# Optimization experiments

Measured on AMD Instinct MI355X. Metric: run time of the kernel, lower is better.

The kernel has to match this reference:

```python
import jax, jax.numpy as jnp
import numpy as np

B, CQ, CR, HID, H, W = 8, 1024, 512, 256, 48, 48


def setup_inputs() -> dict:
    key = jax.random.key(0)
    ks = jax.random.split(key, 6)
    return {
        "query_features": jax.random.normal(ks[0], (B, CQ, H, W), dtype=jnp.float32),
        "reference_features": jax.random.normal(ks[1], (B, CR, H, W), dtype=jnp.float32),
        "Wq": jax.random.normal(ks[2], (HID, CQ), dtype=jnp.float32) * (1.0 / np.sqrt(CQ)),
        "bq": jax.random.normal(ks[3], (HID,), dtype=jnp.float32) * 0.01,
        "Wk": jax.random.normal(ks[4], (HID, CR), dtype=jnp.float32) * (1.0 / np.sqrt(CR)),
        "bk": jax.random.normal(ks[5], (HID,), dtype=jnp.float32) * 0.01,
    }


def reference(query_features, reference_features, Wq, bq, Wk, bk):
    b, _, h1, w1 = query_features.shape
    h2, w2 = reference_features.shape[-2:]
    # 1x1 convs == per-pixel linear projections
    Q = jnp.einsum("oc,bchw->bohw", Wq, query_features) + bq[None, :, None, None]
    K = jnp.einsum("oc,bchw->bohw", Wk, reference_features) + bk[None, :, None, None]
    # V: [b, c_ref, h2*w2]
    V = reference_features.reshape(b, reference_features.shape[1], h2 * w2)
    # attention logits: [b, h1, w1, h2*w2]
    attn = jnp.einsum("bcij,bckl->bijkl", Q, K).reshape(b, h1, w1, h2 * w2)
    attn = jax.nn.softmax(attn, axis=3)
    # weighted sum of V: [b, c_ref, h1, w1]
    attended = jnp.einsum("bijp,bcp->bcij", attn, V)
    return attended
```

## Files before the change

kernel.cpp:

```cpp
#include <hip/hip_runtime.h>

#define BB   8
#define PP   2304
#define CQD  1024
#define CRD  512
#define HIDD 256
#define GB   4
#define NKB  36
#define LOG2E 1.4426950408889634f

typedef float f32x4 __attribute__((ext_vector_type(4)));
typedef __bf16 bf16x8 __attribute__((ext_vector_type(8)));
typedef unsigned short u16x8 __attribute__((ext_vector_type(8)));
typedef unsigned short u16x4 __attribute__((ext_vector_type(4)));
typedef unsigned int u32x4 __attribute__((ext_vector_type(4)));
typedef unsigned short ushort_t;

__device__ __forceinline__ unsigned short f2bf(float f) {
  unsigned int u = __float_as_uint(f);
  u += 0x7fffu + ((u >> 16) & 1u);
  return (unsigned short)(u >> 16);
}
__device__ __forceinline__ float bf2f(unsigned short h) {
  return __uint_as_float(((unsigned int)h) << 16);
}
__device__ __forceinline__ bf16x8 load_bf8(const ushort_t* p) {
  return *(const bf16x8*)p;
}
__device__ __forceinline__ void async16(const void* g, void* l) {
  __builtin_amdgcn_global_load_lds(
      (const __attribute__((address_space(1))) unsigned int*)g,
      (__attribute__((address_space(3))) unsigned int*)l, 16, 0, 0);
}

#define MFMA16(a, b, c) __builtin_amdgcn_mfma_f32_16x16x32_bf16((a), (b), (c), 0, 0, 0)

__global__ __launch_bounds__(256) void wcast_kernel(
    const float* __restrict__ W, ushort_t* __restrict__ Wh,
    ushort_t* __restrict__ Wl) {
  const size_t i = ((size_t)blockIdx.x * 256 + threadIdx.x) * 8;
  float4 a = *(const float4*)(W + i);
  float4 b2 = *(const float4*)(W + i + 4);
  float av[8] = {a.x, a.y, a.z, a.w, b2.x, b2.y, b2.z, b2.w};
  u16x8 h, l;
#pragma unroll
  for (int j = 0; j < 8; ++j) {
    unsigned short hh = f2bf(av[j]);
    h[j] = hh;
    l[j] = f2bf(av[j] - bf2f(hh));
  }
  *(u16x8*)(Wh + i) = h;
  *(u16x8*)(Wl + i) = l;
}

template <int C>
__global__ __launch_bounds__(256) void tcast_kernel(
    const float* __restrict__ X, ushort_t* __restrict__ Th,
    ushort_t* __restrict__ Tl) {
  const int b = blockIdx.z;
  const int p0 = blockIdx.x * 64;
  const int c0 = blockIdx.y * 64;
  const int tid = threadIdx.x;

  __shared__ unsigned int HL[64][66];

  {
    const int cr = tid >> 2;
    const int ch = tid & 3;
    const float* src = X + ((size_t)b * C + c0 + cr) * PP + p0 + ch * 16;
#pragma unroll
    for (int i = 0; i < 4; ++i) {
      float4 v = *(const float4*)(src + i * 4);
      float vv[4] = {v.x, v.y, v.z, v.w};
#pragma unroll
      for (int k = 0; k < 4; ++k) {
        unsigned short h = f2bf(vv[k]);
        unsigned short l = f2bf(vv[k] - bf2f(h));
        HL[ch * 16 + i * 4 + k][cr] =
            (unsigned int)h | ((unsigned int)l << 16);
      }
    }
  }
  __syncthreads();
  {
    const int pr = tid >> 2;
    const int pc = tid & 3;
    u16x8 hv[2], lv[2];
#pragma unroll
    for (int m = 0; m < 2; ++m)
#pragma unroll
      for (int j = 0; j < 8; ++j) {
        unsigned int wb = HL[pr][pc * 16 + m * 8 + j];
        hv[m][j] = (unsigned short)(wb & 0xffffu);
        lv[m][j] = (unsigned short)(wb >> 16);
      }
    const size_t obase = ((size_t)b * PP + p0 + pr) * C + c0 + pc * 16;
    *(u16x8*)(Th + obase) = hv[0];
    *(u16x8*)(Th + obase + 8) = hv[1];
    *(u16x8*)(Tl + obase) = lv[0];
    *(u16x8*)(Tl + obase + 8) = lv[1];
  }
}

template <int C>
__global__ __launch_bounds__(256, 2) void projgemm_kernel(
    const ushort_t* __restrict__ Wh, const ushort_t* __restrict__ Wl,
    const ushort_t* __restrict__ Xh, const ushort_t* __restrict__ Xl,
    const float* __restrict__ bias, ushort_t* __restrict__ Oh,
    ushort_t* __restrict__ Ol) {
  const int bp0 = blockIdx.x * 128;
  const int o0 = blockIdx.y * 128;
  const int tid = threadIdx.x;
  const int lane = tid & 63;
  const int w = tid >> 6;
  const int l15 = lane & 15;
  const int quad = lane >> 4;
  const int wm = w & 1;
  const int wn = w >> 1;

  __shared__ __align__(16) ushort_t AB[2][4][128][32];

  f32x4 acc[4][4] = {};

  const ushort_t* srcs[4] = {Wh + (size_t)o0 * C, Wl + (size_t)o0 * C,
                             Xh + (size_t)bp0 * C, Xl + (size_t)bp0 * C};
  const ushort_t* mysrc = srcs[w];
  const int r16 = lane >> 2;
  const int c8 = (lane & 3) * 8;

  auto stage = [&](int cs, int buf) {
    const ushort_t* sp = mysrc + cs * 32 + c8;
#pragma unroll
    for (int i = 0; i < 8; ++i)
      async16(sp + (size_t)(i * 16 + r16) * C, &AB[buf][w][i * 16][0]);
  };

  stage(0, 0);
  __syncthreads();

  const int NS = C / 32;
  for (int cs = 0; cs < NS; ++cs) {
    const int buf = cs & 1;
    if (cs + 1 < NS) stage(cs + 1, buf ^ 1);

    bf16x8 ah[4], al[4], bh[4], bl[4];
#pragma unroll
    for (int mt = 0; mt < 4; ++mt) {
      const int row = wm * 64 + mt * 16 + l15;
      ah[mt] = load_bf8(&AB[buf][0][row][quad * 8]);
      al[mt] = load_bf8(&AB[buf][1][row][quad * 8]);
    }
#pragma unroll
    for (int nt = 0; nt < 4; ++nt) {
      const int row = wn * 64 + nt * 16 + l15;
      bh[nt] = load_bf8(&AB[buf][2][row][quad * 8]);
      bl[nt] = load_bf8(&AB[buf][3][row][quad * 8]);
    }
#pragma unroll
    for (int mt = 0; mt < 4; ++mt)
#pragma unroll
      for (int nt = 0; nt < 4; ++nt) {
        acc[mt][nt] = MFMA16(ah[mt], bh[nt], acc[mt][nt]);
        acc[mt][nt] = MFMA16(al[mt], bh[nt], acc[mt][nt]);
        acc[mt][nt] = MFMA16(ah[mt], bl[nt], acc[mt][nt]);
      }
    __syncthreads();
  }

#pragma unroll
  for (int mt = 0; mt < 4; ++mt) {
    const int ob = o0 + wm * 64 + mt * 16 + quad * 4;
    float bv[4];
#pragma unroll
    for (int r = 0; r < 4; ++r) bv[r] = bias[ob + r];
#pragma unroll
    for (int nt = 0; nt < 4; ++nt) {
      const int bp = bp0 + wn * 64 + nt * 16 + l15;
      u16x4 hs, ls;
#pragma unroll
      for (int r = 0; r < 4; ++r) {
        float v2 = acc[mt][nt][r] + bv[r];
        unsigned short h = f2bf(v2);
        hs[r] = h;
        ls[r] = f2bf(v2 - bf2f(h));
      }
      const size_t base = (size_t)bp * HIDD + ob;
      *(u16x4*)(Oh + base) = hs;
      *(u16x4*)(Ol + base) = ls;
    }
  }
}

template <int C>
__global__ __launch_bounds__(256) void proj_kernel(
    const float* __restrict__ X, const float* __restrict__ W,
    const float* __restrict__ bias, ushort_t* __restrict__ Oh,
    ushort_t* __restrict__ Ol) {
  const int b = blockIdx.z;
  const int p0 = blockIdx.y * 64;
  const int o0 = blockIdx.x * 64;
  const int tid = threadIdx.x;
  const int lane = tid & 63;
  const int wave = tid >> 6;
  const int wm = wave & 1;
  const int wn = wave >> 1;
  const int l15 = lane & 15;
  const int quad = lane >> 4;

  __shared__ ushort_t Xh[64][40];
  __shared__ ushort_t Xl[64][40];

  f32x4 acc[2][2] = {};
  const float* Xb = X + (size_t)b * C * PP;
  const int cc = tid >> 3;
  const int ppo = (tid & 7) * 8;

  for (int c0 = 0; c0 < C; c0 += 32) {
    const float* src = Xb + (size_t)(c0 + cc) * PP + p0 + ppo;
    float4 v0 = *(const float4*)(src);
    float4 v1 = *(const float4*)(src + 4);
    float vv[8] = {v0.x, v0.y, v0.z, v0.w, v1.x, v1.y, v1.z, v1.w};
#pragma unroll
    for (int j = 0; j < 8; ++j) {
      unsigned short h = f2bf(vv[j]);
      Xh[ppo + j][cc] = h;
      Xl[ppo + j][cc] = f2bf(vv[j] - bf2f(h));
    }
    __syncthreads();

    bf16x8 wh[2], wl[2];
#pragma unroll
    for (int mt = 0; mt < 2; ++mt) {
      const float* wsrc =
          W + (size_t)(o0 + wm * 32 + mt * 16 + l15) * C + c0 + quad * 8;
      float4 a0 = *(const float4*)(wsrc);
      float4 a1 = *(const float4*)(wsrc + 4);
      float av[8] = {a0.x, a0.y, a0.z, a0.w, a1.x, a1.y, a1.z, a1.w};
      u16x8 hh, ll;
#pragma unroll
      for (int j = 0; j < 8; ++j) {
        unsigned short h = f2bf(av[j]);
        hh[j] = h;
        ll[j] = f2bf(av[j] - bf2f(h));
      }
      wh[mt] = __builtin_bit_cast(bf16x8, hh);
      wl[mt] = __builtin_bit_cast(bf16x8, ll);
    }

#pragma unroll
    for (int nt = 0; nt < 2; ++nt) {
      const int pr = wn * 32 + nt * 16 + l15;
      bf16x8 xh = load_bf8(&Xh[pr][quad * 8]);
      bf16x8 xl = load_bf8(&Xl[pr][quad * 8]);
#pragma unroll
      for (int mt = 0; mt < 2; ++mt) {
        acc[mt][nt] = MFMA16(wh[mt], xh, acc[mt][nt]);
        acc[mt][nt] = MFMA16(wl[mt], xh, acc[mt][nt]);
        acc[mt][nt] = MFMA16(wh[mt], xl, acc[mt][nt]);
      }
    }
    __syncthreads();
  }

#pragma unroll
  for (int mt = 0; mt < 2; ++mt) {
    const int ob = o0 + wm * 32 + mt * 16 + quad * 4;
#pragma unroll
    for (int nt = 0; nt < 2; ++nt) {
      const int p = p0 + wn * 32 + nt * 16 + l15;
      u16x4 hs, ls;
#pragma unroll
      for (int r = 0; r < 4; ++r) {
        float v = acc[mt][nt][r] + bias[ob + r];
        unsigned short h = f2bf(v);
        hs[r] = h;
        ls[r] = f2bf(v - bf2f(h));
      }
      const size_t base = ((size_t)b * PP + p) * HIDD + ob;
      *(u16x4*)(Oh + base) = hs;
      *(u16x4*)(Ol + base) = ls;
    }
  }
}

__global__ void cast_v_kernel(const float* __restrict__ X,
                              ushort_t* __restrict__ V) {
  const size_t i = ((size_t)blockIdx.x * 256 + threadIdx.x) * 4;
  float4 v = *(const float4*)(X + i);
  u16x4 o;
  o[0] = f2bf(v.x); o[1] = f2bf(v.y); o[2] = f2bf(v.z); o[3] = f2bf(v.w);
  *(u16x4*)(V + i) = o;
}

__global__ __launch_bounds__(256, 2) void sgemm_kernel(
    const ushort_t* __restrict__ Qh, const ushort_t* __restrict__ Ql,
    const ushort_t* __restrict__ Kh, const ushort_t* __restrict__ Kl,
    ushort_t* __restrict__ Pbuf, float* __restrict__ mpart,
    float* __restrict__ lpart, int bbase) {
  const int b = blockIdx.z;
  const int gb = bbase + b;
  const int q0 = blockIdx.x * 128;
  const int k0 = blockIdx.y * 128;
  const int tid = threadIdx.x;
  const int lane = tid & 63;
  const int w = tid >> 6;
  const int l15 = lane & 15;
  const int quad = lane >> 4;
  const int wm = w & 1;
  const int wn = w >> 1;

  __shared__ __align__(16) ushort_t AB[2][4][128][32];

  f32x4 acc[4][4] = {};

  const ushort_t* srcs[4] = {Qh + ((size_t)gb * PP + q0) * HIDD,
                             Ql + ((size_t)gb * PP + q0) * HIDD,
                             Kh + ((size_t)gb * PP + k0) * HIDD,
                             Kl + ((size_t)gb * PP + k0) * HIDD};
  const ushort_t* mysrc = srcs[w];
  const int r16 = lane >> 2;
  const int c8 = (lane & 3) * 8;

  auto stage = [&](int cs, int buf) {
    const ushort_t* sp = mysrc + cs * 32 + c8;
#pragma unroll
    for (int i = 0; i < 8; ++i)
      async16(sp + (size_t)(i * 16 + r16) * HIDD, &AB[buf][w][i * 16][0]);
  };

  stage(0, 0);
  __syncthreads();

  for (int cs = 0; cs < 8; ++cs) {
    const int buf = cs & 1;
    if (cs + 1 < 8) stage(cs + 1, buf ^ 1);

    bf16x8 ah[4], al[4], bh[4], bl[4];
#pragma unroll
    for (int mt = 0; mt < 4; ++mt) {
      const int row = wm * 64 + mt * 16 + l15;
      ah[mt] = load_bf8(&AB[buf][0][row][quad * 8]);
      al[mt] = load_bf8(&AB[buf][1][row][quad * 8]);
    }
#pragma unroll
    for (int nt = 0; nt < 4; ++nt) {
      const int row = wn * 64 + nt * 16 + l15;
      bh[nt] = load_bf8(&AB[buf][2][row][quad * 8]);
      bl[nt] = load_bf8(&AB[buf][3][row][quad * 8]);
    }
#pragma unroll
    for (int mt = 0; mt < 4; ++mt)
#pragma unroll
      for (int nt = 0; nt < 4; ++nt) {
        acc[mt][nt] = MFMA16(ah[mt], bh[nt], acc[mt][nt]);
        acc[mt][nt] = MFMA16(al[mt], bh[nt], acc[mt][nt]);
        acc[mt][nt] = MFMA16(ah[mt], bl[nt], acc[mt][nt]);
      }
    __syncthreads();
  }

  const int kb = blockIdx.y * 2 + wn;
#pragma unroll
  for (int mt = 0; mt < 4; ++mt) {
#pragma unroll
    for (int r = 0; r < 4; ++r) {
      float m = fmaxf(fmaxf(acc[mt][0][r], acc[mt][1][r]),
                      fmaxf(acc[mt][2][r], acc[mt][3][r]));
      m = fmaxf(m, __shfl_xor(m, 1));
      m = fmaxf(m, __shfl_xor(m, 2));
      m = fmaxf(m, __shfl_xor(m, 4));
      m = fmaxf(m, __shfl_xor(m, 8));
      float p0 = __expf(acc[mt][0][r] - m);
      float p1 = __expf(acc[mt][1][r] - m);
      float p2 = __expf(acc[mt][2][r] - m);
      float p3 = __expf(acc[mt][3][r] - m);
      float e = p0 + p1 + p2 + p3;
      e += __shfl_xor(e, 1);
      e += __shfl_xor(e, 2);
      e += __shfl_xor(e, 4);
      e += __shfl_xor(e, 8);
      const int q = q0 + wm * 64 + mt * 16 + quad * 4 + r;
      ushort_t* prow = Pbuf + ((size_t)b * PP + q) * PP + k0 + wn * 64 + l15;
      prow[0] = f2bf(p0);
      prow[16] = f2bf(p1);
      prow[32] = f2bf(p2);
      prow[48] = f2bf(p3);
      if (l15 == 0) {
        mpart[((size_t)b * NKB + kb) * PP + q] = m;
        lpart[((size_t)b * NKB + kb) * PP + q] = e;
      }
    }
  }
}

__global__ __launch_bounds__(256) void stats_kernel(
    const float* __restrict__ mpart, const float* __restrict__ lpart,
    float* __restrict__ alphab) {
  const int q = blockIdx.x * 256 + threadIdx.x;
  const int b = blockIdx.y;
  float m[NKB];
  float M = -3.0e38f;
#pragma unroll
  for (int kb = 0; kb < NKB; ++kb) {
    m[kb] = mpart[((size_t)b * NKB + kb) * PP + q];
    M = fmaxf(M, m[kb]);
  }
  float L = 0.f;
#pragma unroll
  for (int kb = 0; kb < NKB; ++kb)
    L += __expf(m[kb] - M) * lpart[((size_t)b * NKB + kb) * PP + q];
  const float rL = 1.f / L;
#pragma unroll
  for (int kb = 0; kb < NKB; ++kb)
    alphab[((size_t)b * NKB + kb) * PP + q] = __expf(m[kb] - M) * rL;
}

__global__ __launch_bounds__(256, 2) void pv_kernel(
    const ushort_t* __restrict__ Pb, const ushort_t* __restrict__ Vb,
    const float* __restrict__ alphab, float* __restrict__ out, int bbase) {
  const int b = blockIdx.z;
  const int gb = bbase + b;
  const int m0 = blockIdx.x * 64;
  const int n0 = blockIdx.y * 128;
  const int tid = threadIdx.x;
  const int lane = tid & 63;
  const int w = tid >> 6;
  const int l15 = lane & 15;
  const int quad = lane >> 4;
  const int wm = w & 1;
  const int wn = w >> 1;

  __shared__ __align__(16) ushort_t Plds[2][64][64];
  __shared__ __align__(16) ushort_t Vt[2][128][64];

  f32x4 acc[2][4] = {};

  const ushort_t* P_base = Pb + ((size_t)b * PP + m0) * PP;
  const ushort_t* V_base = Vb + ((size_t)gb * CRD + n0) * PP;
  const float* a_base =
      alphab + (size_t)b * NKB * PP + m0 + wm * 32 + quad * 4;

  const int lr = lane >> 3;
  const int lc = lane & 7;

  auto stage = [&](int kb, int buf) {
#pragma unroll
    for (int j = 0; j < 2; ++j) {
      const int row = w * 16 + j * 8 + lr;
      const int ch = lc ^ (row & 7);
      async16(P_base + (size_t)row * PP + kb * 64 + ch * 8,
              &Plds[buf][w * 16 + j * 8][0]);
    }
#pragma unroll
    for (int j = 0; j < 4; ++j) {
      const int row = w * 32 + j * 8 + lr;
      const int ch = lc ^ (row & 7);
      async16(V_base + (size_t)row * PP + kb * 64 + ch * 8,
              &Vt[buf][w * 32 + j * 8][0]);
    }
  };

  stage(0, 0);
  __syncthreads();

  for (int kb = 0; kb < NKB; ++kb) {
    const int buf = kb & 1;
    if (kb + 1 < NKB) stage(kb + 1, buf ^ 1);

    f32x4 av[2];
#pragma unroll
    for (int mt = 0; mt < 2; ++mt)
      av[mt] = *(const f32x4*)(a_base + (size_t)kb * PP + mt * 16);

    f32x4 pacc[2][4] = {};
#pragma unroll
    for (int h = 0; h < 2; ++h) {
      bf16x8 pa[2], vf[4];
#pragma unroll
      for (int mt = 0; mt < 2; ++mt) {
        const int row = wm * 32 + mt * 16 + l15;
        const int g = (h * 4 + quad) ^ (row & 7);
        pa[mt] = load_bf8(&Plds[buf][row][g * 8]);
      }
#pragma unroll
      for (int nt = 0; nt < 4; ++nt) {
        const int row = wn * 64 + nt * 16 + l15;
        const int g = (h * 4 + quad) ^ (row & 7);
        vf[nt] = load_bf8(&Vt[buf][row][g * 8]);
      }
#pragma unroll
      for (int mt = 0; mt < 2; ++mt)
#pragma unroll
        for (int nt = 0; nt < 4; ++nt)
          pacc[mt][nt] = MFMA16(pa[mt], vf[nt], pacc[mt][nt]);
    }

#pragma unroll
    for (int mt = 0; mt < 2; ++mt)
#pragma unroll
      for (int nt = 0; nt < 4; ++nt)
        acc[mt][nt] += av[mt] * pacc[mt][nt];

    __syncthreads();
  }

#pragma unroll
  for (int mt = 0; mt < 2; ++mt) {
    const int q = m0 + wm * 32 + mt * 16 + quad * 4;
#pragma unroll
    for (int nt = 0; nt < 4; ++nt) {
      const int ch = n0 + wn * 64 + nt * 16 + l15;
      *(f32x4*)(out + ((size_t)gb * CRD + ch) * PP + q) = acc[mt][nt];
    }
  }
}

__global__ __launch_bounds__(256, 2) void attn_direct_kernel(
    const ushort_t* __restrict__ Qh, const ushort_t* __restrict__ Ql,
    const ushort_t* __restrict__ Kh, const ushort_t* __restrict__ Kl,
    const ushort_t* __restrict__ Vb, float* __restrict__ out) {
  const int b = blockIdx.z;
  const int qb = blockIdx.x;
  const int tid = threadIdx.x;
  const int lane = tid & 63;
  const int w = tid >> 6;
  const int l15 = lane & 15;
  const int quad = lane >> 4;

  __shared__ __align__(16) ushort_t Kbuf[2][2][16][520];
  __shared__ __align__(16) ushort_t P_lds[4][16][40];

  bf16x8 qh[8], ql[8];
  {
    const size_t qrow = ((size_t)b * PP + qb * 64 + w * 16 + l15) * HIDD;
#pragma unroll
    for (int ks = 0; ks < 8; ++ks) {
      qh[ks] = load_bf8(Qh + qrow + ks * 32 + quad * 8);
      ql[ks] = load_bf8(Ql + qrow + ks * 32 + quad * 8);
    }
  }

  f32x4 o_acc[32] = {};
  float m_run[4] = {-3.0e38f, -3.0e38f, -3.0e38f, -3.0e38f};
  float l_run[4] = {0.f, 0.f, 0.f, 0.f};

  const ushort_t* Kb[2] = {Kh + (size_t)b * PP * HIDD,
                           Kl + (size_t)b * PP * HIDD};
  const ushort_t* vbase = Vb + ((size_t)b * CRD + l15) * PP + quad * 8;

  auto stage = [&](int t, int buf) {
#pragma unroll
    for (int j = 0; j < 8; ++j) {
      const int idx = w * 8 + j;
      const int hl = idx >> 4;
      const int pair = idx & 15;
      const ushort_t* src =
          Kb[hl] + ((size_t)(t * 32 + pair * 2)) * HIDD + lane * 8;
      async16(src, &Kbuf[buf][hl][pair][0]);
    }
  };

  stage(0, 0);
  __syncthreads();

  for (int t = 0; t < PP / 32; ++t) {
    const int buf = t & 1;
    if (t + 1 < PP / 32) stage(t + 1, buf ^ 1);

    f32x4 sa0 = {}, sa1 = {};
#pragma unroll
    for (int ks = 0; ks < 8; ++ks) {
      const int co = (l15 & 1) * 256 + ks * 32 + quad * 8;
      bf16x8 kh0 = load_bf8(&Kbuf[buf][0][(l15 >> 1)][co]);
      bf16x8 kl0 = load_bf8(&Kbuf[buf][1][(l15 >> 1)][co]);
      bf16x8 kh1 = load_bf8(&Kbuf[buf][0][8 + (l15 >> 1)][co]);
      bf16x8 kl1 = load_bf8(&Kbuf[buf][1][8 + (l15 >> 1)][co]);
      sa0 = MFMA16(qh[ks], kh0, sa0);
      sa1 = MFMA16(qh[ks], kh1, sa1);
      sa0 = MFMA16(ql[ks], kh0, sa0);
      sa1 = MFMA16(ql[ks], kh1, sa1);
      sa0 = MFMA16(qh[ks], kl0, sa0);
      sa1 = MFMA16(qh[ks], kl1, sa1);
    }

    float mx[4], al[4], p0[4], p1[4], rs[4];
#pragma unroll
    for (int r = 0; r < 4; ++r) mx[r] = fmaxf(sa0[r], sa1[r]);
#pragma unroll
    for (int d = 1; d < 16; d <<= 1)
#pragma unroll
      for (int r = 0; r < 4; ++r) mx[r] = fmaxf(mx[r], __shfl_xor(mx[r], d));
#pragma unroll
    for (int r = 0; r < 4; ++r) {
      const float mnew = fmaxf(m_run[r], mx[r]);
      al[r] = __expf(m_run[r] - mnew);
      m_run[r] = mnew;
      p0[r] = __expf(sa0[r] - mnew);
      p1[r] = __expf(sa1[r] - mnew);
      rs[r] = p0[r] + p1[r];
    }
#pragma unroll
    for (int d = 1; d < 16; d <<= 1)
#pragma unroll
      for (int r = 0; r < 4; ++r) rs[r] += __shfl_xor(rs[r], d);
#pragma unroll
    for (int r = 0; r < 4; ++r) l_run[r] = l_run[r] * al[r] + rs[r];

#pragma unroll
    for (int r = 0; r < 4; ++r) {
      P_lds[w][quad * 4 + r][l15] = f2bf(p0[r]);
      P_lds[w][quad * 4 + r][16 + l15] = f2bf(p1[r]);
    }
    asm volatile("s_waitcnt lgkmcnt(0)" ::: "memory");
    bf16x8 pa = load_bf8(&P_lds[w][l15][quad * 8]);

#pragma unroll
    for (int nt = 0; nt < 32; ++nt)
#pragma unroll
      for (int r = 0; r < 4; ++r) o_acc[nt][r] *= al[r];

    const ushort_t* vt = vbase + t * 32;
#pragma unroll
    for (int nt = 0; nt < 32; ++nt) {
      bf16x8 vfr = load_bf8(vt + (size_t)nt * 16 * PP);
      o_acc[nt] = MFMA16(pa, vfr, o_acc[nt]);
    }
    __syncthreads();
  }

  float rl[4];
#pragma unroll
  for (int r = 0; r < 4; ++r) rl[r] = 1.f / l_run[r];
  const int q0 = qb * 64 + w * 16 + quad * 4;
#pragma unroll
  for (int nt = 0; nt < 32; ++nt) {
    const int c = nt * 16 + l15;
    float* op = out + ((size_t)b * CRD + c) * PP + q0;
#pragma unroll
    for (int r = 0; r < 4; ++r) op[r] = o_acc[nt][r] * rl[r];
  }
}

extern "C" void kernel_launch(void* const* d_in, const int* in_sizes, int n_in,
                              void* d_out, int out_size, void* d_ws,
                              size_t ws_size, hipStream_t stream) {
  (void)in_sizes; (void)n_in; (void)out_size;

  const float* Xq = (const float*)d_in[0];
  const float* Xr = (const float*)d_in[1];
  const float* Wq = (const float*)d_in[2];
  const float* bq = (const float*)d_in[3];
  const float* Wk = (const float*)d_in[4];
  const float* bk = (const float*)d_in[5];
  float* out = (float*)d_out;

  const size_t nQK = (size_t)BB * PP * HIDD;
  const size_t nV = (size_t)BB * CRD * PP;

  ushort_t* p = (ushort_t*)d_ws;
  ushort_t* Qh = p; p += nQK;
  ushort_t* Ql = p; p += nQK;
  ushort_t* Kh = p; p += nQK;
  ushort_t* Kl = p; p += nQK;
  ushort_t* Vb = p; p += nV;
  ushort_t* scratch = p;

  ushort_t* Pbuf = scratch;
  float* mpart = (float*)(Pbuf + (size_t)GB * PP * PP);
  float* lpart = mpart + (size_t)GB * NKB * PP;
  float* alphab = lpart + (size_t)GB * NKB * PP;
  char* attn_end = (char*)(alphab + (size_t)GB * NKB * PP);

  ushort_t* Xth = scratch;
  ushort_t* Xtl = Xth + (size_t)BB * PP * CQD;
  ushort_t* Wh2 = Xtl + (size_t)BB * PP * CQD;
  ushort_t* Wl2 = Wh2 + (size_t)HIDD * CQD;
  char* proj_end = (char*)(Wl2 + (size_t)HIDD * CQD);

  char* endp = proj_end > attn_end ? proj_end : attn_end;
  const size_t needed = (size_t)(endp - (char*)d_ws);

  if (ws_size >= needed) {
    cast_v_kernel<<<dim3(nV / 1024), 256, 0, stream>>>(Xr, Vb);

    wcast_kernel<<<dim3(HIDD * CQD / 2048), 256, 0, stream>>>(Wq, Wh2, Wl2);
    tcast_kernel<CQD><<<dim3(PP / 64, CQD / 64, BB), 256, 0, stream>>>(
        Xq, Xth, Xtl);
    projgemm_kernel<CQD><<<dim3(BB * PP / 128, HIDD / 128), 256, 0, stream>>>(
        Wh2, Wl2, Xth, Xtl, bq, Qh, Ql);

    wcast_kernel<<<dim3(HIDD * CRD / 2048), 256, 0, stream>>>(Wk, Wh2, Wl2);
    tcast_kernel<CRD><<<dim3(PP / 64, CRD / 64, BB), 256, 0, stream>>>(
        Xr, Xth, Xtl);
    projgemm_kernel<CRD><<<dim3(BB * PP / 128, HIDD / 128), 256, 0, stream>>>(
        Wh2, Wl2, Xth, Xtl, bk, Kh, Kl);

    for (int g = 0; g < BB / GB; ++g) {
      const int bbase = g * GB;
      sgemm_kernel<<<dim3(PP / 128, PP / 128, GB), 256, 0, stream>>>(
          Qh, Ql, Kh, Kl, Pbuf, mpart, lpart, bbase);
      stats_kernel<<<dim3(PP / 256, GB), 256, 0, stream>>>(mpart, lpart,
                                                           alphab);
      pv_kernel<<<dim3(PP / 64, CRD / 128, GB), 256, 0, stream>>>(
          Pbuf, Vb, alphab, out, bbase);
    }
  } else {
    proj_kernel<CQD><<<dim3(4, PP / 64, BB), 256, 0, stream>>>(Xq, Wq, bq, Qh,
                                                               Ql);
    proj_kernel<CRD><<<dim3(4, PP / 64, BB), 256, 0, stream>>>(Xr, Wk, bk, Kh,
                                                               Kl);
    cast_v_kernel<<<dim3(nV / 1024), 256, 0, stream>>>(Xr, Vb);
    attn_direct_kernel<<<dim3(PP / 64, 1, BB), 256, 0, stream>>>(
        Qh, Ql, Kh, Kl, Vb, out);
  }
}
```

Before: 511.4 us.

## Stage P tile through LDS for coalesced stores, remap blocks for XCDs, fuse V cast

The sgemm epilogue now writes the bf16 probability tile into swizzled shared memory and then stores full 16-byte rows to global memory, replacing scattered 2-byte stores. Both sgemm and pv remap the linear block index so that neighbouring tiles are grouped per XCD (stride 8), aiming for better L2 locality. The separate V cast kernel is folded into the reference-feature transpose cast, removing one pass over the reference features. pv_kernel launch bounds go from 2 to 3 blocks per CU, which may raise register pressure.

```diff
diff --git a/kernel.cpp b/kernel.cpp
--- a/kernel.cpp
+++ b/kernel.cpp
@@ -53,10 +53,10 @@
   *(u16x8*)(Wl + i) = l;
 }
 
-template <int C>
+template <int C, bool WV>
 __global__ __launch_bounds__(256) void tcast_kernel(
     const float* __restrict__ X, ushort_t* __restrict__ Th,
-    ushort_t* __restrict__ Tl) {
+    ushort_t* __restrict__ Tl, ushort_t* __restrict__ Vb) {
   const int b = blockIdx.z;
   const int p0 = blockIdx.x * 64;
   const int c0 = blockIdx.y * 64;
@@ -68,6 +68,7 @@
     const int cr = tid >> 2;
     const int ch = tid & 3;
     const float* src = X + ((size_t)b * C + c0 + cr) * PP + p0 + ch * 16;
+    u16x8 vcast[2];
 #pragma unroll
     for (int i = 0; i < 4; ++i) {
       float4 v = *(const float4*)(src + i * 4);
@@ -78,7 +79,13 @@
         unsigned short l = f2bf(vv[k] - bf2f(h));
         HL[ch * 16 + i * 4 + k][cr] =
             (unsigned int)h | ((unsigned int)l << 16);
-      }
+        if (WV) vcast[i >> 1][(i & 1) * 4 + k] = h;
+      }
+    }
+    if (WV) {
+      ushort_t* vd = Vb + ((size_t)b * C + c0 + cr) * PP + p0 + ch * 16;
+      *(u16x8*)(vd) = vcast[0];
+      *(u16x8*)(vd + 8) = vcast[1];
     }
   }
   __syncthreads();
@@ -297,10 +304,14 @@
     const ushort_t* __restrict__ Kh, const ushort_t* __restrict__ Kl,
     ushort_t* __restrict__ Pbuf, float* __restrict__ mpart,
     float* __restrict__ lpart, int bbase) {
-  const int b = blockIdx.z;
+  const int lin = blockIdx.x + 18 * blockIdx.y + 324 * blockIdx.z;
+  const int o = (lin & 7) * 162 + (lin >> 3);
+  const int b = o / 324;
+  const int rem = o % 324;
+  const int q0 = (rem % 18) * 128;
+  const int k0 = (rem / 18) * 128;
+
   const int gb = bbase + b;
-  const int q0 = blockIdx.x * 128;
-  const int k0 = blockIdx.y * 128;
   const int tid = threadIdx.x;
   const int lane = tid & 63;
   const int w = tid >> 6;
@@ -359,7 +370,8 @@
     __syncthreads();
   }
 
-  const int kb = blockIdx.y * 2 + wn;
+  ushort_t* Pt = (ushort_t*)&AB[0][0][0][0];
+  const int kb = (k0 >> 6) + wn;
 #pragma unroll
   for (int mt = 0; mt < 4; ++mt) {
 #pragma unroll
@@ -379,16 +391,33 @@
       e += __shfl_xor(e, 2);
       e += __shfl_xor(e, 4);
       e += __shfl_xor(e, 8);
-      const int q = q0 + wm * 64 + mt * 16 + quad * 4 + r;
-      ushort_t* prow = Pbuf + ((size_t)b * PP + q) * PP + k0 + wn * 64 + l15;
-      prow[0] = f2bf(p0);
-      prow[16] = f2bf(p1);
-      prow[32] = f2bf(p2);
-      prow[48] = f2bf(p3);
+      const int row = wm * 64 + mt * 16 + quad * 4 + r;
+      const int rx = row & 15;
+      ushort_t* ptrow = Pt + row * 128;
+      float pv[4] = {p0, p1, p2, p3};
+#pragma unroll
+      for (int nt = 0; nt < 4; ++nt) {
+        const int col = wn * 64 + nt * 16 + l15;
+        ptrow[(((col >> 3) ^ rx) << 3) + (col & 7)] = f2bf(pv[nt]);
+      }
       if (l15 == 0) {
+        const int q = q0 + row;
         mpart[((size_t)b * NKB + kb) * PP + q] = m;
         lpart[((size_t)b * NKB + kb) * PP + q] = e;
       }
+    }
+  }
+  __syncthreads();
+  {
+    const int row = tid >> 1;
+    const int half = tid & 1;
+    const int rx = row & 15;
+    const ushort_t* srcr = Pt + row * 128;
+    ushort_t* dst = Pbuf + ((size_t)b * PP + q0 + row) * PP + k0 + half * 64;
+#pragma unroll
+    for (int j = 0; j < 8; ++j) {
+      u16x8 v = *(const u16x8*)(srcr + (((half * 8 + j) ^ rx) << 3));
+      *(u16x8*)(dst + j * 8) = v;
     }
   }
 }
@@ -415,13 +444,16 @@
     alphab[((size_t)b * NKB + kb) * PP + q] = __expf(m[kb] - M) * rL;
 }
 
-__global__ __launch_bounds__(256, 2) void pv_kernel(
+__global__ __launch_bounds__(256, 3) void pv_kernel(
     const ushort_t* __restrict__ Pb, const ushort_t* __restrict__ Vb,
     const float* __restrict__ alphab, float* __restrict__ out, int bbase) {
-  const int b = blockIdx.z;
+  const int lin = blockIdx.x + 36 * blockIdx.y + 144 * blockIdx.z;
+  const int o = (lin & 7) * 72 + (lin >> 3);
+  const int b = o / 144;
+  const int m0 = (o % 36) * 64;
+  const int n0 = ((o / 36) % 4) * 128;
+
   const int gb = bbase + b;
-  const int m0 = blockIdx.x * 64;
-  const int n0 = blockIdx.y * 128;
   const int tid = threadIdx.x;
   const int lane = tid & 63;
   const int w = tid >> 6;
@@ -681,17 +713,15 @@
   const size_t needed = (size_t)(endp - (char*)d_ws);
 
   if (ws_size >= needed) {
-    cast_v_kernel<<<dim3(nV / 1024), 256, 0, stream>>>(Xr, Vb);
-
     wcast_kernel<<<dim3(HIDD * CQD / 2048), 256, 0, stream>>>(Wq, Wh2, Wl2);
-    tcast_kernel<CQD><<<dim3(PP / 64, CQD / 64, BB), 256, 0, stream>>>(
-        Xq, Xth, Xtl);
+    tcast_kernel<CQD, false><<<dim3(PP / 64, CQD / 64, BB), 256, 0, stream>>>(
+        Xq, Xth, Xtl, nullptr);
     projgemm_kernel<CQD><<<dim3(BB * PP / 128, HIDD / 128), 256, 0, stream>>>(
         Wh2, Wl2, Xth, Xtl, bq, Qh, Ql);
 
     wcast_kernel<<<dim3(HIDD * CRD / 2048), 256, 0, stream>>>(Wk, Wh2, Wl2);
-    tcast_kernel<CRD><<<dim3(PP / 64, CRD / 64, BB), 256, 0, stream>>>(
-        Xr, Xth, Xtl);
+    tcast_kernel<CRD, true><<<dim3(PP / 64, CRD / 64, BB), 256, 0, stream>>>(
+        Xr, Xth, Xtl, Vb);
     projgemm_kernel<CRD><<<dim3(BB * PP / 128, HIDD / 128), 256, 0, stream>>>(
         Wh2, Wl2, Xth, Xtl, bk, Kh, Kl);
 
```

Measured after the change: 490.1 us. 4.2% less time.
